# Kernel tuning notes

Measured on AMD Instinct MI355X. Metric: run time of the kernel, lower is better.

Reference implementation:

```python
import jax, jax.numpy as jnp
import numpy as np

N_NODES = 200000   # node frontier pool size per layer
N_ENT = 10000
BATCH = 256
N_LAYER = 3
N_EDGES = 1000000
REL_VOCAB = 402    # 2*n_rel + 2 with n_rel=200
HID = 20


def setup_inputs() -> dict:
    key = jax.random.key(0)
    ks = jax.random.split(key, 12)
    return {
        "query_rel": jax.random.randint(ks[0], (BATCH,), 0, REL_VOCAB, dtype=jnp.int32),
        "src_idx": jax.random.randint(ks[1], (N_LAYER, N_EDGES), 0, N_NODES, dtype=jnp.int32),
        "rel_idx": jax.random.randint(ks[2], (N_LAYER, N_EDGES), 0, REL_VOCAB, dtype=jnp.int32),
        "batch_idx": jax.random.randint(ks[3], (N_LAYER, N_EDGES), 0, BATCH, dtype=jnp.int32),
        "dst_idx": jax.random.randint(ks[4], (N_LAYER, N_EDGES), 0, N_NODES, dtype=jnp.int32),
        "final_batch": jax.random.randint(ks[5], (N_NODES,), 0, BATCH, dtype=jnp.int32),
        "final_ent": jax.random.randint(ks[6], (N_NODES,), 0, N_ENT, dtype=jnp.int32),
        "rela_embed": jax.random.normal(ks[7], (REL_VOCAB, HID), dtype=jnp.float32),
        "W1": jax.random.normal(ks[8], (30, 60), dtype=jnp.float32) * 0.1,
        "W2": jax.random.normal(ks[9], (1, 30), dtype=jnp.float32) * 0.1,
        "Wc": jax.random.normal(ks[10], (1, HID), dtype=jnp.float32) * 0.1,
        "bc": jnp.zeros((1,), dtype=jnp.float32),
    }


def reference(query_rel, src_idx, rel_idx, batch_idx, dst_idx,
              final_batch, final_ent, rela_embed, W1, W2, Wc, bc):
    q_emb_all = rela_embed[query_rel]  # [B, 20] query relation embedding per batch query

    def layer(hidden, edges):
        src, rel, bidx, dst = edges
        h_src = hidden[src]            # [E, 20] gather current node states
        r_emb = rela_embed[rel]        # [E, 20]
        q_emb = q_emb_all[bidx]        # [E, 20]
        attn_in = jnp.concatenate([h_src, r_emb, q_emb], axis=1)  # [E, 60]
        # attention MLP: sigmoid(W2 @ relu(W1 @ x)), 60 -> 30 -> 1
        score = jax.nn.sigmoid(jax.nn.relu(attn_in @ W1.T) @ W2.T)  # [E, 1]
        msg = score * (h_src + r_emb)  # [E, 20] embed_rel weighted by attention
        # sparse attention-weighted aggregation (torch.sparse.mm)
        new_hidden = jax.ops.segment_sum(msg, dst, num_segments=N_NODES)
        return new_hidden, None

    hidden0 = jnp.zeros((N_NODES, HID), dtype=rela_embed.dtype)
    hidden, _ = jax.lax.scan(layer, hidden0, (src_idx, rel_idx, batch_idx, dst_idx))

    result = (hidden @ Wc.T + bc).reshape(-1)  # [N_NODES] linear classifier
    score_all = jnp.zeros((BATCH, N_ENT), dtype=result.dtype)
    score_all = score_all.at[final_batch, final_ent].set(result)
    return score_all
```

## Files before the change

kernel.cpp:

```cpp
#include <hip/hip_runtime.h>
#include <hip/hip_bf16.h>
#include <hip/hip_fp16.h>

#define N_NODES 200000
#define N_ENT   10000
#define BATCH   256
#define N_LAYER 3
#define N_EDGES 1000000
#define REL_VOCAB 402
#define HID 20
#define CAP 32
#define HPADH 32

__global__ __launch_bounds__(256) void tables_kernel(
    const float* __restrict__ W1, const float* __restrict__ rela,
    const int* __restrict__ query_rel,
    float* __restrict__ R1T, float* __restrict__ Q1T)
{
    int t = blockIdx.x * blockDim.x + threadIdx.x;
    if (t < 30 * REL_VOCAB) {
        int j = t / REL_VOCAB, r = t % REL_VOCAB;
        const float* w  = W1 + j * 60 + 20;
        const float* re = rela + (size_t)r * HID;
        float a = 0.f;
        #pragma unroll
        for (int k = 0; k < HID; ++k) a = fmaf(w[k], re[k], a);
        R1T[t] = a;
    } else if (t < 30 * REL_VOCAB + 30 * BATCH) {
        int u = t - 30 * REL_VOCAB;
        int j = u / BATCH, b = u % BATCH;
        int qr = query_rel[b];
        const float* w  = W1 + j * 60 + 40;
        const float* qe = rela + (size_t)qr * HID;
        float a = 0.f;
        #pragma unroll
        for (int k = 0; k < HID; ++k) a = fmaf(w[k], qe[k], a);
        Q1T[j * BATCH + b] = a;
    }
}

__global__ __launch_bounds__(256) void score0_kernel(
    const float* __restrict__ R1T, const float* __restrict__ Q1T,
    const float* __restrict__ W2, float* __restrict__ score0)
{
    int t = blockIdx.x * blockDim.x + threadIdx.x;
    if (t >= BATCH * REL_VOCAB) return;
    int b = t / REL_VOCAB, r = t % REL_VOCAB;
    float hs = 0.f;
    #pragma unroll 5
    for (int j = 0; j < 30; ++j) {
        float v = R1T[j * REL_VOCAB + r] + Q1T[j * BATCH + b];
        hs = fmaf(W2[j], fmaxf(v, 0.f), hs);
    }
    score0[t] = 1.f / (1.f + __expf(-hs));
}

template<int LAYER>
__global__ __launch_bounds__(256) void msg_rec_kernel(
    const int* __restrict__ src, const int* __restrict__ rel,
    const int* __restrict__ bidx, const int* __restrict__ dst,
    const __half* __restrict__ h16,
    const float* __restrict__ W1, const float* __restrict__ W2,
    const float* __restrict__ R1T, const float* __restrict__ Q1T,
    const float* __restrict__ score0,
    int* __restrict__ cnt, uint2* __restrict__ recs)
{
    int e = blockIdx.x * blockDim.x + threadIdx.x;
    if (e >= N_EDGES) return;
    const int r = rel[e];
    const int b = bidx[e];
    const int d = dst[e];

    float score;
    unsigned int srec = 0;
    if (LAYER == 0) {
        score = score0[b * REL_VOCAB + r];
    } else {
        const int s = src[e];
        srec = (unsigned int)s;
        float hv[HID];
        const uint2* hp = reinterpret_cast<const uint2*>(h16 + (size_t)s * HPADH);
        #pragma unroll
        for (int c = 0; c < 5; ++c) {
            uint2 v = hp[c];
            __half2 a0 = *reinterpret_cast<__half2*>(&v.x);
            __half2 a1 = *reinterpret_cast<__half2*>(&v.y);
            float2 f0 = __half22float2(a0), f1 = __half22float2(a1);
            hv[4*c+0] = f0.x; hv[4*c+1] = f0.y; hv[4*c+2] = f1.x; hv[4*c+3] = f1.y;
        }
        float hs = 0.f;
        #pragma unroll 3
        for (int j = 0; j < 30; ++j) {
            float t = R1T[j * REL_VOCAB + r] + Q1T[j * BATCH + b];
            const float* w = W1 + j * 60;
            #pragma unroll
            for (int k = 0; k < HID; ++k) t = fmaf(w[k], hv[k], t);
            hs = fmaf(W2[j], fmaxf(t, 0.f), hs);
        }
        score = 1.f / (1.f + __expf(-hs));
    }

    int pos = atomicAdd(&cnt[d], 1);
    if (pos < CAP) {
        __half sc = __float2half(score);
        unsigned int lo = (unsigned int)(unsigned short)r |
                          ((unsigned int)__half_as_ushort(sc) << 16);
        recs[(size_t)d * CAP + pos] = make_uint2(srec, lo);
    }
}

template<int LAYER>
__global__ __launch_bounds__(256) void gather_rec_kernel(
    const int* __restrict__ cnt, const uint2* __restrict__ recs,
    const __half* __restrict__ h16_in,
    const float* __restrict__ rela,
    __half* __restrict__ h16_out,
    float* __restrict__ hF_out)
{
    int tid = blockIdx.x * blockDim.x + threadIdx.x;
    if (tid >= N_NODES * 5) return;
    const int d = tid / 5;
    const int c = tid % 5;
    int n = cnt[d];
    if (n > CAP) n = CAP;

    const uint2* rp = recs + (size_t)d * CAP;
    float4 acc = make_float4(0.f, 0.f, 0.f, 0.f);
    for (int i = 0; i < n; ++i) {
        uint2 rec = rp[i];
        const int r = (int)(rec.y & 0xFFFFu);
        const float score = __half2float(__ushort_as_half((unsigned short)(rec.y >> 16)));
        float4 rv = *reinterpret_cast<const float4*>(rela + (size_t)r * HID + c * 4);
        float4 m = rv;
        if (LAYER != 0) {
            const int s = (int)rec.x;
            uint2 hvv = *reinterpret_cast<const uint2*>(h16_in + (size_t)s * HPADH + c * 4);
            __half2 a0 = *reinterpret_cast<__half2*>(&hvv.x);
            __half2 a1 = *reinterpret_cast<__half2*>(&hvv.y);
            float2 f0 = __half22float2(a0), f1 = __half22float2(a1);
            m.x += f0.x; m.y += f0.y; m.z += f1.x; m.w += f1.y;
        }
        acc.x = fmaf(score, m.x, acc.x);
        acc.y = fmaf(score, m.y, acc.y);
        acc.z = fmaf(score, m.z, acc.z);
        acc.w = fmaf(score, m.w, acc.w);
    }

    if (LAYER == 2) {
        reinterpret_cast<float4*>(hF_out)[(size_t)d * 5 + c] = acc;
    } else {
        __half2 p0 = __floats2half2_rn(acc.x, acc.y);
        __half2 p1 = __floats2half2_rn(acc.z, acc.w);
        uint2 w = make_uint2(*reinterpret_cast<unsigned int*>(&p0),
                             *reinterpret_cast<unsigned int*>(&p1));
        *reinterpret_cast<uint2*>(h16_out + (size_t)d * HPADH + c * 4) = w;
    }
}

__global__ __launch_bounds__(256) void winner_kernel(
    const int* __restrict__ final_batch, const int* __restrict__ final_ent,
    int* __restrict__ winner)
{
    int i = blockIdx.x * blockDim.x + threadIdx.x;
    if (i >= N_NODES) return;
    const int slot = final_batch[i] * N_ENT + final_ent[i];
    atomicMax(&winner[slot], i);
}

__global__ __launch_bounds__(256) void out_kernel(
    const int* __restrict__ winner,
    const float* __restrict__ hidden,
    const float* __restrict__ Wc, const float* __restrict__ bc,
    float* __restrict__ out)
{
    int sidx = blockIdx.x * blockDim.x + threadIdx.x;
    if (sidx >= BATCH * N_ENT) return;
    const int w = winner[sidx];
    float v = 0.0f;
    if (w >= 0) {
        const float4* hp = reinterpret_cast<const float4*>(hidden + (size_t)w * HID);
        float acc = bc[0];
        #pragma unroll
        for (int k = 0; k < 5; ++k) {
            float4 h = hp[k];
            acc = fmaf(h.x, Wc[4*k+0], acc);
            acc = fmaf(h.y, Wc[4*k+1], acc);
            acc = fmaf(h.z, Wc[4*k+2], acc);
            acc = fmaf(h.w, Wc[4*k+3], acc);
        }
        v = acc;
    }
    out[sidx] = v;
}

template<bool FIRST>
__global__ __launch_bounds__(256) void edge_kernel(
    const int* __restrict__ src, const int* __restrict__ rel,
    const int* __restrict__ bidx, const int* __restrict__ dst,
    const int* __restrict__ query_rel,
    const float* __restrict__ hidden_in, float* __restrict__ hidden_out,
    const float* __restrict__ rela_embed,
    const float* __restrict__ W1, const float* __restrict__ W2)
{
    int e = blockIdx.x * blockDim.x + threadIdx.x;
    if (e >= N_EDGES) return;
    const int s = src[e];
    const int r = rel[e];
    const int b = bidx[e];
    const int d = dst[e];
    const int qr = query_rel[b];
    float x[60];
    if (FIRST) {
        #pragma unroll
        for (int k = 0; k < HID; ++k) x[k] = 0.0f;
    } else {
        const float4* hp = reinterpret_cast<const float4*>(hidden_in + (size_t)s * HID);
        #pragma unroll
        for (int k = 0; k < 5; ++k) {
            float4 v = hp[k];
            x[4*k+0] = v.x; x[4*k+1] = v.y; x[4*k+2] = v.z; x[4*k+3] = v.w;
        }
    }
    {
        const float4* rp = reinterpret_cast<const float4*>(rela_embed + (size_t)r * HID);
        #pragma unroll
        for (int k = 0; k < 5; ++k) {
            float4 v = rp[k];
            x[20+4*k+0] = v.x; x[20+4*k+1] = v.y; x[20+4*k+2] = v.z; x[20+4*k+3] = v.w;
        }
    }
    {
        const float4* qp = reinterpret_cast<const float4*>(rela_embed + (size_t)qr * HID);
        #pragma unroll
        for (int k = 0; k < 5; ++k) {
            float4 v = qp[k];
            x[40+4*k+0] = v.x; x[40+4*k+1] = v.y; x[40+4*k+2] = v.z; x[40+4*k+3] = v.w;
        }
    }
    float hsum = 0.0f;
    #pragma unroll 2
    for (int j = 0; j < 30; ++j) {
        float acc = 0.0f;
        const float* w1row = W1 + j * 60;
        #pragma unroll
        for (int k = (FIRST ? HID : 0); k < 60; ++k)
            acc = fmaf(w1row[k], x[k], acc);
        hsum = fmaf(W2[j], fmaxf(acc, 0.0f), hsum);
    }
    const float score = 1.0f / (1.0f + __expf(-hsum));
    float* outp = hidden_out + (size_t)d * HID;
    #pragma unroll
    for (int k = 0; k < HID; ++k) {
        const float m = FIRST ? (score * x[20+k]) : (score * (x[k] + x[20+k]));
        atomicAdd(outp + k, m);
    }
}

__global__ __launch_bounds__(256) void outF_kernel(
    const int* __restrict__ winner,
    const float* __restrict__ hidden,
    const float* __restrict__ Wc, const float* __restrict__ bc,
    float* __restrict__ out)
{
    int sidx = blockIdx.x * blockDim.x + threadIdx.x;
    if (sidx >= BATCH * N_ENT) return;
    const int w = winner[sidx];
    float v = 0.0f;
    if (w >= 0) {
        const float4* hp = reinterpret_cast<const float4*>(hidden + (size_t)w * HID);
        float acc = bc[0];
        #pragma unroll
        for (int k = 0; k < 5; ++k) {
            float4 h = hp[k];
            acc = fmaf(h.x, Wc[4*k+0], acc);
            acc = fmaf(h.y, Wc[4*k+1], acc);
            acc = fmaf(h.z, Wc[4*k+2], acc);
            acc = fmaf(h.w, Wc[4*k+3], acc);
        }
        v = acc;
    }
    out[sidx] = v;
}

extern "C" void kernel_launch(void* const* d_in, const int* in_sizes, int n_in,
                              void* d_out, int out_size, void* d_ws, size_t ws_size,
                              hipStream_t stream) {
    const int*   query_rel   = (const int*)  d_in[0];
    const int*   src_idx     = (const int*)  d_in[1];
    const int*   rel_idx     = (const int*)  d_in[2];
    const int*   batch_idx   = (const int*)  d_in[3];
    const int*   dst_idx     = (const int*)  d_in[4];
    const int*   final_batch = (const int*)  d_in[5];
    const int*   final_ent   = (const int*)  d_in[6];
    const float* rela_embed  = (const float*)d_in[7];
    const float* W1          = (const float*)d_in[8];
    const float* W2          = (const float*)d_in[9];
    const float* Wc          = (const float*)d_in[10];
    const float* bc          = (const float*)d_in[11];
    float* out = (float*)d_out;

    const size_t HF_B   = (size_t)N_NODES * HID * sizeof(float);
    const size_t H16P_B = (size_t)N_NODES * HPADH * sizeof(__half);
    const size_t REC_B  = (size_t)N_NODES * CAP * sizeof(uint2);
    const size_t CNT_B  = (size_t)N_LAYER * N_NODES * sizeof(int);
    const size_t R1T_B  = ((size_t)30 * REL_VOCAB * sizeof(float) + 255) & ~255ull;
    const size_t Q1T_B  = ((size_t)30 * BATCH * sizeof(float) + 255) & ~255ull;
    const size_t SC0_B  = ((size_t)BATCH * REL_VOCAB * sizeof(float) + 255) & ~255ull;
    const size_t WIN_B  = (size_t)BATCH * N_ENT * sizeof(int);

    const size_t REQ = HF_B + 2*H16P_B + REC_B + CNT_B + R1T_B + Q1T_B + SC0_B + WIN_B;

    const int EDGE_BLOCKS = (N_EDGES + 255) / 256;
    const int NODE_BLOCKS = (N_NODES + 255) / 256;
    const int GATH_BLOCKS = (N_NODES * 5 + 255) / 256;

    char* ws = (char*)d_ws;

    if (ws_size >= REQ) {
        size_t o = 0;
        float*  hF     = (float*) (ws + o); o += HF_B;
        __half* h16A   = (__half*)(ws + o); o += H16P_B;
        __half* h16B   = (__half*)(ws + o); o += H16P_B;
        uint2*  recs   = (uint2*) (ws + o); o += REC_B;
        int*    cnt    = (int*)   (ws + o); o += CNT_B;
        float*  R1T    = (float*) (ws + o); o += R1T_B;
        float*  Q1T    = (float*) (ws + o); o += Q1T_B;
        float*  score0 = (float*) (ws + o); o += SC0_B;
        int*    winner = (int*)   (ws + o); o += WIN_B;

        tables_kernel<<<(30*REL_VOCAB + 30*BATCH + 255)/256, 256, 0, stream>>>(
            W1, rela_embed, query_rel, R1T, Q1T);
        score0_kernel<<<(BATCH*REL_VOCAB + 255)/256, 256, 0, stream>>>(
            R1T, Q1T, W2, score0);
        hipMemsetAsync(cnt, 0, CNT_B, stream);

        {
            int* cntL = cnt;
            msg_rec_kernel<0><<<EDGE_BLOCKS, 256, 0, stream>>>(
                src_idx, rel_idx, batch_idx, dst_idx,
                nullptr, W1, W2, R1T, Q1T, score0, cntL, recs);
            gather_rec_kernel<0><<<GATH_BLOCKS, 256, 0, stream>>>(
                cntL, recs, nullptr, rela_embed, h16A, nullptr);
        }
        {
            int* cntL = cnt + N_NODES;
            msg_rec_kernel<1><<<EDGE_BLOCKS, 256, 0, stream>>>(
                src_idx + (size_t)N_EDGES, rel_idx + (size_t)N_EDGES,
                batch_idx + (size_t)N_EDGES, dst_idx + (size_t)N_EDGES,
                h16A, W1, W2, R1T, Q1T, score0, cntL, recs);
            gather_rec_kernel<1><<<GATH_BLOCKS, 256, 0, stream>>>(
                cntL, recs, h16A, rela_embed, h16B, nullptr);
        }
        {
            int* cntL = cnt + 2 * N_NODES;
            msg_rec_kernel<2><<<EDGE_BLOCKS, 256, 0, stream>>>(
                src_idx + 2*(size_t)N_EDGES, rel_idx + 2*(size_t)N_EDGES,
                batch_idx + 2*(size_t)N_EDGES, dst_idx + 2*(size_t)N_EDGES,
                h16B, W1, W2, R1T, Q1T, score0, cntL, recs);
            gather_rec_kernel<2><<<GATH_BLOCKS, 256, 0, stream>>>(
                cntL, recs, h16B, rela_embed, nullptr, hF);
        }

        hipMemsetAsync(winner, 0xFF, WIN_B, stream);
        winner_kernel<<<NODE_BLOCKS, 256, 0, stream>>>(final_batch, final_ent, winner);
        out_kernel<<<(BATCH * N_ENT + 255) / 256, 256, 0, stream>>>(winner, hF, Wc, bc, out);
    } else {
        float* hiddenA = (float*)(ws);
        float* hiddenB = (float*)(ws + HF_B);
        int*   winner  = (int*)  (ws + 2 * HF_B);

        hipMemsetAsync(hiddenA, 0, HF_B, stream);
        edge_kernel<true><<<EDGE_BLOCKS, 256, 0, stream>>>(
            src_idx, rel_idx, batch_idx, dst_idx,
            query_rel, nullptr, hiddenA, rela_embed, W1, W2);

        hipMemsetAsync(hiddenB, 0, HF_B, stream);
        edge_kernel<false><<<EDGE_BLOCKS, 256, 0, stream>>>(
            src_idx + (size_t)N_EDGES, rel_idx + (size_t)N_EDGES,
            batch_idx + (size_t)N_EDGES, dst_idx + (size_t)N_EDGES,
            query_rel, hiddenA, hiddenB, rela_embed, W1, W2);

        hipMemsetAsync(hiddenA, 0, HF_B, stream);
        edge_kernel<false><<<EDGE_BLOCKS, 256, 0, stream>>>(
            src_idx + 2*(size_t)N_EDGES, rel_idx + 2*(size_t)N_EDGES,
            batch_idx + 2*(size_t)N_EDGES, dst_idx + 2*(size_t)N_EDGES,
            query_rel, hiddenB, hiddenA, rela_embed, W1, W2);

        hipMemsetAsync(winner, 0xFF, (size_t)BATCH * N_ENT * sizeof(int), stream);
        winner_kernel<<<NODE_BLOCKS, 256, 0, stream>>>(final_batch, final_ent, winner);
        outF_kernel<<<(BATCH * N_ENT + 255) / 256, 256, 0, stream>>>(winner, hiddenA, Wc, bc, out);
    }
}
```

Baseline: 324.6 us.

## Partition edges by destination slice to localize atomics per XCD

Adds a partition pass that buckets each layer's edges into 8 destination-node slices, with 32 sub-buckets per slice. The message and gather kernels then map block IDs so that each slice's work lands on one XCD, assuming round-robin block dispatch across the 8 XCDs. The goal is to keep per-destination atomic counters and record writes within one XCD's L2 rather than scattering them across all chiplets. In exchange it adds an extra pass that reads and writes 16-byte records per edge, plus a fixed bucket capacity that silently drops edges if a bucket overflows.

After: 392.8 us. 1.21x slower.

```diff
diff --git a/kernel.cpp b/kernel.cpp
--- a/kernel.cpp
+++ b/kernel.cpp
@@ -12,6 +12,12 @@
 #define CAP 32
 #define HPADH 32
 
+#define NXCD   8
+#define SLICE_N 25000
+#define NSUB   32
+#define CAPP   5120
+#define EPB    16
+
 __global__ __launch_bounds__(256) void tables_kernel(
     const float* __restrict__ W1, const float* __restrict__ rela,
     const int* __restrict__ query_rel,
@@ -55,72 +61,125 @@
     score0[t] = 1.f / (1.f + __expf(-hs));
 }
 
-template<int LAYER>
-__global__ __launch_bounds__(256) void msg_rec_kernel(
+__global__ __launch_bounds__(256) void part_kernel(
     const int* __restrict__ src, const int* __restrict__ rel,
     const int* __restrict__ bidx, const int* __restrict__ dst,
+    int* __restrict__ pcnt,
+    uint4* __restrict__ recsP)
+{
+    __shared__ int lhist[NXCD];
+    __shared__ int lbase[NXCD];
+    const int t  = threadIdx.x;
+    const int sub = blockIdx.x % NSUB;
+    const int e0 = blockIdx.x * (256 * EPB);
+
+    if (t < NXCD) lhist[t] = 0;
+    __syncthreads();
+
+    int rank[EPB];
+    #pragma unroll
+    for (int j = 0; j < EPB; ++j) {
+        const int e = e0 + j * 256 + t;
+        if (e < N_EDGES) {
+            const int d = dst[e];
+            rank[j] = atomicAdd(&lhist[d / SLICE_N], 1);
+        }
+    }
+    __syncthreads();
+    if (t < NXCD) {
+        const int c = lhist[t];
+        lbase[t] = (c > 0) ? atomicAdd(&pcnt[t * NSUB + sub], c) : 0;
+    }
+    __syncthreads();
+
+    #pragma unroll
+    for (int j = 0; j < EPB; ++j) {
+        const int e = e0 + j * 256 + t;
+        if (e >= N_EDGES) continue;
+        const int d   = dst[e];
+        const int bin = d / SLICE_N;
+        const int pos = lbase[bin] + rank[j];
+        if (pos < CAPP)
+            recsP[(size_t)(bin * NSUB + sub) * CAPP + pos] =
+                make_uint4((unsigned int)src[e],
+                           (unsigned int)rel[e] | ((unsigned int)bidx[e] << 16),
+                           (unsigned int)d, 0u);
+    }
+}
+
+template<int LAYER>
+__global__ __launch_bounds__(256) void msgX_kernel(
+    const uint4* __restrict__ recsP, const int* __restrict__ pcnt,
     const __half* __restrict__ h16,
     const float* __restrict__ W1, const float* __restrict__ W2,
     const float* __restrict__ R1T, const float* __restrict__ Q1T,
     const float* __restrict__ score0,
     int* __restrict__ cnt, uint2* __restrict__ recs)
 {
-    int e = blockIdx.x * blockDim.x + threadIdx.x;
-    if (e >= N_EDGES) return;
-    const int r = rel[e];
-    const int b = bidx[e];
-    const int d = dst[e];
-
-    float score;
-    unsigned int srec = 0;
-    if (LAYER == 0) {
-        score = score0[b * REL_VOCAB + r];
-    } else {
-        const int s = src[e];
-        srec = (unsigned int)s;
-        float hv[HID];
-        const uint2* hp = reinterpret_cast<const uint2*>(h16 + (size_t)s * HPADH);
-        #pragma unroll
-        for (int c = 0; c < 5; ++c) {
-            uint2 v = hp[c];
-            __half2 a0 = *reinterpret_cast<__half2*>(&v.x);
-            __half2 a1 = *reinterpret_cast<__half2*>(&v.y);
-            float2 f0 = __half22float2(a0), f1 = __half22float2(a1);
-            hv[4*c+0] = f0.x; hv[4*c+1] = f0.y; hv[4*c+2] = f1.x; hv[4*c+3] = f1.y;
-        }
-        float hs = 0.f;
-        #pragma unroll 3
-        for (int j = 0; j < 30; ++j) {
-            float t = R1T[j * REL_VOCAB + r] + Q1T[j * BATCH + b];
-            const float* w = W1 + j * 60;
+    const int bin   = blockIdx.x & 7;
+    const int sub   = (blockIdx.x >> 3) & (NSUB - 1);
+    const int slice = blockIdx.x >> 8;
+    int m = pcnt[bin * NSUB + sub];
+    if (m > CAPP) m = CAPP;
+    const uint4* seg = recsP + (size_t)(bin * NSUB + sub) * CAPP;
+
+    for (int p = slice * 256 + threadIdx.x; p < m; p += 2048) {
+        const uint4 pr = seg[p];
+        const int s = (int)pr.x;
+        const int r = (int)(pr.y & 0xFFFFu);
+        const int b = (int)(pr.y >> 16);
+        const int d = (int)pr.z;
+
+        float score;
+        if (LAYER == 0) {
+            score = score0[b * REL_VOCAB + r];
+        } else {
+            float hv[HID];
+            const uint2* hp = reinterpret_cast<const uint2*>(h16 + (size_t)s * HPADH);
             #pragma unroll
-            for (int k = 0; k < HID; ++k) t = fmaf(w[k], hv[k], t);
-            hs = fmaf(W2[j], fmaxf(t, 0.f), hs);
-        }
-        score = 1.f / (1.f + __expf(-hs));
-    }
-
-    int pos = atomicAdd(&cnt[d], 1);
-    if (pos < CAP) {
-        __half sc = __float2half(score);
-        unsigned int lo = (unsigned int)(unsigned short)r |
-                          ((unsigned int)__half_as_ushort(sc) << 16);
-        recs[(size_t)d * CAP + pos] = make_uint2(srec, lo);
+            for (int c = 0; c < 5; ++c) {
+                uint2 v = hp[c];
+                __half2 a0 = *reinterpret_cast<__half2*>(&v.x);
+                __half2 a1 = *reinterpret_cast<__half2*>(&v.y);
+                float2 f0 = __half22float2(a0), f1 = __half22float2(a1);
+                hv[4*c+0] = f0.x; hv[4*c+1] = f0.y; hv[4*c+2] = f1.x; hv[4*c+3] = f1.y;
+            }
+            float hs = 0.f;
+            #pragma unroll 3
+            for (int j = 0; j < 30; ++j) {
+                float tt = R1T[j * REL_VOCAB + r] + Q1T[j * BATCH + b];
+                const float* w = W1 + j * 60;
+                #pragma unroll
+                for (int k = 0; k < HID; ++k) tt = fmaf(w[k], hv[k], tt);
+                hs = fmaf(W2[j], fmaxf(tt, 0.f), hs);
+            }
+            score = 1.f / (1.f + __expf(-hs));
+        }
+
+        int pos = atomicAdd(&cnt[d], 1);
+        if (pos < CAP) {
+            __half sc = __float2half(score);
+            unsigned int lo = (unsigned int)(unsigned short)r |
+                              ((unsigned int)__half_as_ushort(sc) << 16);
+            recs[(size_t)d * CAP + pos] = make_uint2(pr.x, lo);
+        }
     }
 }
 
 template<int LAYER>
-__global__ __launch_bounds__(256) void gather_rec_kernel(
+__global__ __launch_bounds__(256) void gatherX_kernel(
     const int* __restrict__ cnt, const uint2* __restrict__ recs,
     const __half* __restrict__ h16_in,
     const float* __restrict__ rela,
     __half* __restrict__ h16_out,
     float* __restrict__ hF_out)
 {
-    int tid = blockIdx.x * blockDim.x + threadIdx.x;
-    if (tid >= N_NODES * 5) return;
-    const int d = tid / 5;
-    const int c = tid % 5;
+    const int bin  = blockIdx.x & 7;
+    const int part = blockIdx.x >> 3;
+    const int u = part * 256 + threadIdx.x;
+    if (u >= SLICE_N * 5) return;
+    const int d = bin * SLICE_N + u / 5;
+    const int c = u % 5;
     int n = cnt[d];
     if (n > CAP) n = CAP;
 
@@ -299,20 +358,25 @@
     const float* bc          = (const float*)d_in[11];
     float* out = (float*)d_out;
 
-    const size_t HF_B   = (size_t)N_NODES * HID * sizeof(float);
-    const size_t H16P_B = (size_t)N_NODES * HPADH * sizeof(__half);
-    const size_t REC_B  = (size_t)N_NODES * CAP * sizeof(uint2);
-    const size_t CNT_B  = (size_t)N_LAYER * N_NODES * sizeof(int);
-    const size_t R1T_B  = ((size_t)30 * REL_VOCAB * sizeof(float) + 255) & ~255ull;
-    const size_t Q1T_B  = ((size_t)30 * BATCH * sizeof(float) + 255) & ~255ull;
-    const size_t SC0_B  = ((size_t)BATCH * REL_VOCAB * sizeof(float) + 255) & ~255ull;
-    const size_t WIN_B  = (size_t)BATCH * N_ENT * sizeof(int);
-
-    const size_t REQ = HF_B + 2*H16P_B + REC_B + CNT_B + R1T_B + Q1T_B + SC0_B + WIN_B;
+    const size_t HF_B    = (size_t)N_NODES * HID * sizeof(float);
+    const size_t H16P_B  = (size_t)N_NODES * HPADH * sizeof(__half);
+    const size_t REC_B   = (size_t)N_NODES * CAP * sizeof(uint2);
+    const size_t RECSP_B = (size_t)NXCD * NSUB * CAPP * sizeof(uint4);
+    const size_t CNT_B   = (size_t)N_LAYER * N_NODES * sizeof(int);
+    const size_t PCNT_B  = ((size_t)N_LAYER * NXCD * NSUB * sizeof(int) + 255) & ~255ull;
+    const size_t R1T_B   = ((size_t)30 * REL_VOCAB * sizeof(float) + 255) & ~255ull;
+    const size_t Q1T_B   = ((size_t)30 * BATCH * sizeof(float) + 255) & ~255ull;
+    const size_t SC0_B   = ((size_t)BATCH * REL_VOCAB * sizeof(float) + 255) & ~255ull;
+    const size_t WIN_B   = (size_t)BATCH * N_ENT * sizeof(int);
+
+    const size_t REQ = HF_B + 2*H16P_B + REC_B + RECSP_B + CNT_B + PCNT_B
+                     + R1T_B + Q1T_B + SC0_B + WIN_B;
 
     const int EDGE_BLOCKS = (N_EDGES + 255) / 256;
     const int NODE_BLOCKS = (N_NODES + 255) / 256;
-    const int GATH_BLOCKS = (N_NODES * 5 + 255) / 256;
+    const int PART_BLOCKS = (N_EDGES + 256*EPB - 1) / (256*EPB);
+    const int MSGX_BLOCKS = NXCD * NSUB * 8;
+    const int GATX_BLOCKS = NXCD * ((SLICE_N * 5 + 255) / 256);
 
     char* ws = (char*)d_ws;
 
@@ -322,7 +386,9 @@
         __half* h16A   = (__half*)(ws + o); o += H16P_B;
         __half* h16B   = (__half*)(ws + o); o += H16P_B;
         uint2*  recs   = (uint2*) (ws + o); o += REC_B;
+        uint4*  recsP  = (uint4*) (ws + o); o += RECSP_B;
         int*    cnt    = (int*)   (ws + o); o += CNT_B;
+        int*    pcnt   = (int*)   (ws + o); o += PCNT_B;
         float*  R1T    = (float*) (ws + o); o += R1T_B;
         float*  Q1T    = (float*) (ws + o); o += Q1T_B;
         float*  score0 = (float*) (ws + o); o += SC0_B;
@@ -333,32 +399,34 @@
         score0_kernel<<<(BATCH*REL_VOCAB + 255)/256, 256, 0, stream>>>(
             R1T, Q1T, W2, score0);
         hipMemsetAsync(cnt, 0, CNT_B, stream);
-
-        {
-            int* cntL = cnt;
-            msg_rec_kernel<0><<<EDGE_BLOCKS, 256, 0, stream>>>(
-                src_idx, rel_idx, batch_idx, dst_idx,
-                nullptr, W1, W2, R1T, Q1T, score0, cntL, recs);
-            gather_rec_kernel<0><<<GATH_BLOCKS, 256, 0, stream>>>(
-                cntL, recs, nullptr, rela_embed, h16A, nullptr);
-        }
-        {
-            int* cntL = cnt + N_NODES;
-            msg_rec_kernel<1><<<EDGE_BLOCKS, 256, 0, stream>>>(
-                src_idx + (size_t)N_EDGES, rel_idx + (size_t)N_EDGES,
-                batch_idx + (size_t)N_EDGES, dst_idx + (size_t)N_EDGES,
-                h16A, W1, W2, R1T, Q1T, score0, cntL, recs);
-            gather_rec_kernel<1><<<GATH_BLOCKS, 256, 0, stream>>>(
-                cntL, recs, h16A, rela_embed, h16B, nullptr);
-        }
-        {
-            int* cntL = cnt + 2 * N_NODES;
-            msg_rec_kernel<2><<<EDGE_BLOCKS, 256, 0, stream>>>(
-                src_idx + 2*(size_t)N_EDGES, rel_idx + 2*(size_t)N_EDGES,
-                batch_idx + 2*(size_t)N_EDGES, dst_idx + 2*(size_t)N_EDGES,
-                h16B, W1, W2, R1T, Q1T, score0, cntL, recs);
-            gather_rec_kernel<2><<<GATH_BLOCKS, 256, 0, stream>>>(
-                cntL, recs, h16B, rela_embed, nullptr, hF);
+        hipMemsetAsync(pcnt, 0, (size_t)N_LAYER * NXCD * NSUB * sizeof(int), stream);
+
+        for (int L = 0; L < N_LAYER; ++L) {
+            const int* src = src_idx   + (size_t)L * N_EDGES;
+            const int* rel = rel_idx   + (size_t)L * N_EDGES;
+            const int* bix = batch_idx + (size_t)L * N_EDGES;
+            const int* dst = dst_idx   + (size_t)L * N_EDGES;
+            int* cntL  = cnt  + (size_t)L * N_NODES;
+            int* pcntL = pcnt + (size_t)L * NXCD * NSUB;
+
+            part_kernel<<<PART_BLOCKS, 256, 0, stream>>>(src, rel, bix, dst, pcntL, recsP);
+
+            if (L == 0) {
+                msgX_kernel<0><<<MSGX_BLOCKS, 256, 0, stream>>>(
+                    recsP, pcntL, nullptr, W1, W2, R1T, Q1T, score0, cntL, recs);
+                gatherX_kernel<0><<<GATX_BLOCKS, 256, 0, stream>>>(
+                    cntL, recs, nullptr, rela_embed, h16A, nullptr);
+            } else if (L == 1) {
+                msgX_kernel<1><<<MSGX_BLOCKS, 256, 0, stream>>>(
+                    recsP, pcntL, h16A, W1, W2, R1T, Q1T, score0, cntL, recs);
+                gatherX_kernel<1><<<GATX_BLOCKS, 256, 0, stream>>>(
+                    cntL, recs, h16A, rela_embed, h16B, nullptr);
+            } else {
+                msgX_kernel<2><<<MSGX_BLOCKS, 256, 0, stream>>>(
+                    recsP, pcntL, h16B, W1, W2, R1T, Q1T, score0, cntL, recs);
+                gatherX_kernel<2><<<GATX_BLOCKS, 256, 0, stream>>>(
+                    cntL, recs, h16B, rela_embed, nullptr, hF);
+            }
         }
 
         hipMemsetAsync(winner, 0xFF, WIN_B, stream);
```
